# Kernel optimization log

Hardware: AMD Instinct MI355X
Metric: run time of the kernel (lower is better)

The kernel has to match this reference:

```python
import jax, jax.numpy as jnp
import numpy as np

BT = 64  # time chunk size (matches Triton BT)


def _chunk_simple_gla(q, k, v, g):
    """Chunked simple-GLA / RWKV6c forward.
    q,k: [B,H,T,K]; v: [B,H,T,V]; g: [B,H,T] per-token log decay.
    Token-level math: S_t = exp(g_t)*S_{t-1} + k_t v_t^T ; o_t = scale * q_t @ S_t.
    Computed chunk-wise exactly as the Triton kernels do.
    """
    B, H, T, K = q.shape
    V = v.shape[-1]
    NT = T // BT
    scale = K ** -0.5

    qc = q.reshape(B, H, NT, BT, K)
    kc = k.reshape(B, H, NT, BT, K)
    vc = v.reshape(B, H, NT, BT, V)
    gc = jnp.cumsum(g.reshape(B, H, NT, BT), axis=-1)  # chunk-local cumulative log decay
    g_last = gc[..., -1]                               # [B,H,NT]

    # per-chunk kv contribution: sum_s k_s (v_s * exp(g_last - g_s))^T
    w = jnp.exp(g_last[..., None] - gc)                # [B,H,NT,BT]
    chunk_kv = jnp.einsum('bhntk,bhntv->bhnkv', kc, vc * w[..., None])
    decay = jnp.exp(g_last)                            # [B,H,NT]

    # inter-chunk state recurrence: h_n = state BEFORE chunk n
    def scan_fn(S, x):
        d, kv = x
        S_new = d[..., None, None] * S + kv
        return S_new, S  # emit state entering this chunk

    xs = (jnp.moveaxis(decay, 2, 0), jnp.moveaxis(chunk_kv, 2, 0))
    S0 = jnp.zeros((B, H, K, V), dtype=q.dtype)
    _, h = jax.lax.scan(scan_fn, S0, xs)               # h: [NT,B,H,K,V]
    h = jnp.moveaxis(h, 0, 2)                          # [B,H,NT,K,V]

    # inter-chunk output: exp(g_t) * q_t @ h_chunk * scale
    o_inter = jnp.einsum('bhntk,bhnkv->bhntv', qc, h) * jnp.exp(gc)[..., None] * scale

    # intra-chunk causal output with gated mask exp(g_i - g_j), i >= j
    s = jnp.einsum('bhnik,bhnjk->bhnij', qc, kc)
    mask = jnp.tril(jnp.ones((BT, BT), dtype=bool))
    s = jnp.where(mask, s * jnp.exp(gc[..., :, None] - gc[..., None, :]) * scale, 0.0)
    o_intra = jnp.einsum('bhnij,bhnjv->bhniv', s, vc)

    return (o_inter + o_intra).reshape(B, H, T, V)


def setup_inputs() -> dict:
    key = jax.random.key(0)
    kq, kk, kv, kg = jax.random.split(key, 4)
    B, H, T, K, V = 2, 32, 4096, 128, 128
    q = jax.random.normal(kq, (B, H, T, K), dtype=jnp.float32)
    k = jax.random.normal(kk, (B, H, T, K), dtype=jnp.float32)
    v = jax.random.normal(kv, (B, H, T, V), dtype=jnp.float32)
    # log-decay gates: negative so exp(cumsum) is bounded (RWKV6/GLA semantics)
    g = -0.5 * jax.random.uniform(kg, (B, H, T), dtype=jnp.float32)
    return {"q": q, "k": k, "v": v, "g": g}


def reference(q, k, v, g):
    return _chunk_simple_gla(q, k, v, g)
```

## Files before the change

kernel.cpp:

```cpp
#include <hip/hip_runtime.h>
#include <hip/hip_bf16.h>


#define BT 64
#define KD 128
#define VD 128
#define VSG 32
#define NCHUNK 64
#define TLEN 4096
#define SCALE 0.08838834764831845f

#define QSTR 136
#define SHSTR 72
#define SVSTR 136
#define VTSTR 72

typedef __bf16 bf16;
typedef __bf16 bf16x8 __attribute__((ext_vector_type(8)));
typedef __bf16 bf16x4 __attribute__((ext_vector_type(4)));
typedef float f32x4 __attribute__((ext_vector_type(4)));

#define MFMA __builtin_amdgcn_mfma_f32_16x16x32_bf16
#define LGKM_BARRIER() do { asm volatile("s_waitcnt lgkmcnt(0)" ::: "memory"); \
                            __builtin_amdgcn_s_barrier(); } while (0)

__device__ __forceinline__ int ksw(int t) { return ((t >> 3) & 3) << 5; }

__device__ __forceinline__ int vt_off(int vc, int t) {
  int byte = vc * (VTSTR * 2) + t * 2;
  byte ^= ((vc >> 2) & 7) << 4;
  return byte >> 1;
}

__device__ __forceinline__ bf16x8 frag_row(const bf16* p, int stride, int row0,
                                           int kk0, int lane) {
  int row = row0 + (lane & 15);
  int kk = kk0 + ((lane >> 4) << 3);
  return *(const bf16x8*)(p + row * stride + kk);
}

__device__ __forceinline__ bf16x8 krow_frag(const bf16* ks_, int row0, int kk0,
                                            int lane) {
  int row = row0 + (lane & 15);
  int kk = kk0 + ((lane >> 4) << 3);
  int byte = (row * (QSTR * 2) + kk * 2) ^ ksw(row);
  return *(const bf16x8*)((const char*)ks_ + byte);
}

__device__ __forceinline__ bf16x8 kcol_frag(const bf16* ks_, int T0, int kdA) {
  int C = ((T0 >> 3) & 3) << 5;
  int b0 = T0 * (QSTR * 2) + kdA * 2;
  bf16x8 f;
#pragma unroll
  for (int j = 0; j < 8; ++j)
    f[j] = *(const bf16*)((const char*)ks_ + ((b0 + j * (QSTR * 2)) ^ C));
  return f;
}

__device__ __forceinline__ void st4(bf16* p, float a, float b, float c, float d) {
  bf16x4 t;
  t[0] = (bf16)a; t[1] = (bf16)b; t[2] = (bf16)c; t[3] = (bf16)d;
  *(bf16x4*)p = t;
}

__global__ void __launch_bounds__(512, 2)
gla_fused(const float* __restrict__ qg, const float* __restrict__ kg,
          const float* __restrict__ vg, const float* __restrict__ gg,
          float* __restrict__ og)
{
  __shared__ __align__(16) bf16 q_s[2][BT * QSTR];
  __shared__ __align__(16) bf16 k_s[2][BT * QSTR];
  __shared__ __align__(16) bf16 vT_s[3][VSG * VTSTR];
  __shared__ __align__(16) bf16 vwT_s[3][VSG * VTSTR];
  __shared__ __align__(16) bf16 sh_s[2][BT * SHSTR];
  __shared__ __align__(16) bf16 svt_s[2][VSG * SVSTR];
  __shared__ __align__(16) float gc_all[NCHUNK][BT];
  __shared__ float glast_all[NCHUNK];

  const int tid = threadIdx.x;
  const int wave = tid >> 6;
  const int lane = tid & 63;
  const int bh = blockIdx.x & 63;
  const int vseg = blockIdx.x >> 6;

  const int jc = lane & 15;
  const int g4 = lane >> 4;
  const int r0 = g4 << 2;

  const int it = wave & 3;
  const int nt = wave >> 2;
  const int jt0 = (wave < 4) ? 0 : 2;

  const size_t qkbase = (size_t)bh * TLEN * KD;
  const size_t gbase = (size_t)bh * TLEN;
  const size_t vbase = (size_t)bh * TLEN * VD + (size_t)vseg * VSG;
  const int vrow = tid >> 3;
  const int vc0 = (tid & 7) << 2;

  float4 qpf[4], kpf[4], vpf;

  auto loadpf = [&](int n) {
    const float4* q4 = (const float4*)(qg + qkbase + (size_t)n * (BT * KD));
    const float4* k4 = (const float4*)(kg + qkbase + (size_t)n * (BT * KD));
#pragma unroll
    for (int i = 0; i < 4; ++i) { qpf[i] = q4[i * 512 + tid]; kpf[i] = k4[i * 512 + tid]; }
    vpf = *(const float4*)(vg + vbase + (size_t)(n * BT + vrow) * VD + vc0);
  };

  auto stage = [&](int b2, int b3, int n) {
#pragma unroll
    for (int i = 0; i < 4; ++i) {
      int f4 = i * 512 + tid;
      int t = f4 >> 5;
      int kd0 = (f4 & 31) << 2;
      st4(&q_s[b2][t * QSTR + kd0], qpf[i].x, qpf[i].y, qpf[i].z, qpf[i].w);
      int byte = (t * (QSTR * 2) + kd0 * 2) ^ ksw(t);
      st4((bf16*)((char*)k_s[b2] + byte), kpf[i].x, kpf[i].y, kpf[i].z, kpf[i].w);
    }
    bf16* vt = vT_s[b3];
    bf16* vwt = vwT_s[b3];
    float wv = __expf(glast_all[n] - gc_all[n][vrow]);
    vt[vt_off(vc0 + 0, vrow)] = (bf16)vpf.x;
    vt[vt_off(vc0 + 1, vrow)] = (bf16)vpf.y;
    vt[vt_off(vc0 + 2, vrow)] = (bf16)vpf.z;
    vt[vt_off(vc0 + 3, vrow)] = (bf16)vpf.w;
    vwt[vt_off(vc0 + 0, vrow)] = (bf16)(vpf.x * wv);
    vwt[vt_off(vc0 + 1, vrow)] = (bf16)(vpf.y * wv);
    vwt[vt_off(vc0 + 2, vrow)] = (bf16)(vpf.z * wv);
    vwt[vt_off(vc0 + 3, vrow)] = (bf16)(vpf.w * wv);
  };

  auto o_emit = [&](int no, int b2o, int b3o, const bf16x8 (&afp)[4]) {
    f32x4 oacc = {0.f, 0.f, 0.f, 0.f};
#pragma unroll
    for (int ks = 0; ks < 4; ++ks) {
      bf16x8 b = frag_row(svt_s[b2o], SVSTR, nt * 16, ks * 32, lane);
      oacc = MFMA(afp[ks], b, oacc, 0, 0, 0);
    }
    {
      float4 e4 = *(const float4*)&gc_all[no][it * 16 + r0];
      const float* ep = (const float*)&e4;
#pragma unroll
      for (int r = 0; r < 4; ++r) oacc[r] *= __expf(ep[r]) * SCALE;
    }
#pragma unroll
    for (int ks = 0; ks < 2; ++ks) {
      bf16x8 a = frag_row(sh_s[b2o], SHSTR, it * 16, ks * 32, lane);
      bf16x8 b = *(const bf16x8*)(vT_s[b3o] + vt_off(nt * 16 + jc, ks * 32 + (g4 << 3)));
      oacc = MFMA(a, b, oacc, 0, 0, 0);
    }
#pragma unroll
    for (int r = 0; r < 4; ++r) {
      int row = it * 16 + r0 + r;
      og[vbase + (size_t)(no * BT + row) * VD + nt * 16 + jc] = oacc[r];
    }
  };

  f32x4 Sa = {0.f, 0.f, 0.f, 0.f}, Sb = {0.f, 0.f, 0.f, 0.f};
  bf16x8 afp[4];

  loadpf(0);
#pragma unroll 1
  for (int i = 0; i < 8; ++i) {
    int cn = wave * 8 + i;
    float a = gg[gbase + cn * BT + lane];
#pragma unroll
    for (int off = 1; off < 64; off <<= 1) {
      float t = __shfl_up(a, off);
      if (lane >= off) a += t;
    }
    gc_all[cn][lane] = a;
    if (lane == 63) glast_all[cn] = a;
  }
  LGKM_BARRIER();
  stage(0, 0, 0);
  loadpf(1);
  LGKM_BARRIER();

  int b3 = 0;
#pragma unroll 1
  for (int n = 0; n < NCHUNK; ++n) {
    const int b2 = n & 1;
    const int b3n = (b3 == 2) ? 0 : b3 + 1;
    const int b3p = (b3 == 0) ? 2 : b3 - 1;

    if (n > 0) o_emit(n - 1, b2 ^ 1, b3p, afp);

    bf16x8 af[4];
#pragma unroll
    for (int ks = 0; ks < 4; ++ks)
      af[ks] = frag_row(q_s[b2], QSTR, it * 16, ks * 32, lane);

    f32x4 sa0 = {0.f,0.f,0.f,0.f}, sa1 = {0.f,0.f,0.f,0.f};
#pragma unroll
    for (int ks = 0; ks < 4; ++ks) {
      bf16x8 a0 = krow_frag(k_s[b2], jt0 * 16, ks * 32, lane);
      bf16x8 a1 = krow_frag(k_s[b2], (jt0 + 1) * 16, ks * 32, lane);
      sa0 = MFMA(a0, af[ks], sa0, 0, 0, 0);
      sa1 = MFMA(a1, af[ks], sa1, 0, 0, 0);
    }
    {
      int i0 = it * 16 + jc;
      float gci = gc_all[n][i0];
#pragma unroll
      for (int t = 0; t < 2; ++t) {
        f32x4 sv = t ? sa1 : sa0;
        int jb = (jt0 + t) * 16 + r0;
        float4 g4v = *(const float4*)&gc_all[n][jb];
        const float* gj = (const float*)&g4v;
        bf16x4 pk;
#pragma unroll
        for (int r = 0; r < 4; ++r) {
          float val = (i0 >= jb + r) ? sv[r] * __expf(gci - gj[r]) * SCALE : 0.f;
          pk[r] = (bf16)val;
        }
        *(bf16x4*)&sh_s[b2][i0 * SHSTR + jb] = pk;
      }
    }

    st4(&svt_s[b2][jc * SVSTR + wave * 16 + r0], Sa[0], Sa[1], Sa[2], Sa[3]);
    st4(&svt_s[b2][(16 + jc) * SVSTR + wave * 16 + r0], Sb[0], Sb[1], Sb[2], Sb[3]);
    {
      float dec = __expf(glast_all[n]);
#pragma unroll
      for (int r = 0; r < 4; ++r) { Sa[r] *= dec; Sb[r] *= dec; }
#pragma unroll
      for (int ks = 0; ks < 2; ++ks) {
        bf16x8 a = kcol_frag(k_s[b2], ks * 32 + (g4 << 3), wave * 16 + jc);
        bf16x8 b0 = *(const bf16x8*)(vwT_s[b3] + vt_off(jc, ks * 32 + (g4 << 3)));
        bf16x8 b1 = *(const bf16x8*)(vwT_s[b3] + vt_off(16 + jc, ks * 32 + (g4 << 3)));
        Sa = MFMA(a, b0, Sa, 0, 0, 0);
        Sb = MFMA(a, b1, Sb, 0, 0, 0);
      }
    }

    if (n + 1 < NCHUNK) {
      stage(b2 ^ 1, b3n, n + 1);
      if (n + 2 < NCHUNK) loadpf(n + 2);
    }

#pragma unroll
    for (int ks = 0; ks < 4; ++ks) afp[ks] = af[ks];
    b3 = b3n;

    LGKM_BARRIER();
  }

  o_emit(NCHUNK - 1, 1, 0, afp);
}

extern "C" void kernel_launch(void* const* d_in, const int* in_sizes, int n_in,
                              void* d_out, int out_size, void* d_ws, size_t ws_size,
                              hipStream_t stream) {
  const float* q = (const float*)d_in[0];
  const float* k = (const float*)d_in[1];
  const float* v = (const float*)d_in[2];
  const float* g = (const float*)d_in[3];
  float* o = (float*)d_out;
  dim3 grid(256);
  dim3 block(512);
  gla_fused<<<grid, block, 0, stream>>>(q, k, v, g, o);
}
```

Baseline: 161.9 us.

## Split sequence into segments with precomputed segment KV states

```diff
diff --git a/kernel.cpp b/kernel.cpp
--- a/kernel.cpp
+++ b/kernel.cpp
@@ -7,6 +7,7 @@
 #define VD 128
 #define VSG 32
 #define NCHUNK 64
+#define SEGC 16
 #define TLEN 4096
 #define SCALE 0.08838834764831845f
 
@@ -14,6 +15,11 @@
 #define SHSTR 72
 #define SVSTR 136
 #define VTSTR 72
+
+#define KV_PER 16384
+#define KV_TOT (64 * 3 * KV_PER)
+#define GS_OFF KV_TOT
+#define WS_NEED ((size_t)(KV_TOT + 192) * 4)
 
 typedef __bf16 bf16;
 typedef __bf16 bf16x8 __attribute__((ext_vector_type(8)));
@@ -61,6 +67,335 @@
   bf16x4 t;
   t[0] = (bf16)a; t[1] = (bf16)b; t[2] = (bf16)c; t[3] = (bf16)d;
   *(bf16x4*)p = t;
+}
+
+__device__ __forceinline__ void st8(bf16* p, const float4& a, const float4& b) {
+  bf16x8 t;
+  t[0] = (bf16)a.x; t[1] = (bf16)a.y; t[2] = (bf16)a.z; t[3] = (bf16)a.w;
+  t[4] = (bf16)b.x; t[5] = (bf16)b.y; t[6] = (bf16)b.z; t[7] = (bf16)b.w;
+  *(bf16x8*)p = t;
+}
+
+__global__ void __launch_bounds__(512, 2)
+gla_pre(const float* __restrict__ kg, const float* __restrict__ vg,
+        const float* __restrict__ gg, float* __restrict__ ws)
+{
+  __shared__ __align__(16) bf16 k_s[2][BT * QSTR];
+  __shared__ __align__(16) bf16 vwT_s[2][VD * VTSTR];
+  __shared__ __align__(16) float gc_all[SEGC][BT];
+  __shared__ float glast_all[SEGC];
+
+  const int tid = threadIdx.x;
+  const int wave = tid >> 6;
+  const int lane = tid & 63;
+  const int bh = blockIdx.x & 63;
+  const int sub = blockIdx.x >> 6;
+
+  const int jc = lane & 15;
+  const int g4 = lane >> 4;
+  const int r0 = g4 << 2;
+
+  const size_t kbase = (size_t)bh * TLEN * KD + (size_t)sub * 1024 * KD;
+  const size_t gbase = (size_t)bh * TLEN + (size_t)sub * 1024;
+  const int vrow = tid >> 3;
+  const int vcq = (tid & 7) << 2;
+
+  float4 kpf[4], vpf[4];
+
+  auto loadall = [&](int n) {
+    const float4* k4 = (const float4*)(kg + kbase + (size_t)n * (BT * KD));
+    kpf[0] = k4[2 * tid];        kpf[1] = k4[2 * tid + 1];
+    kpf[2] = k4[1024 + 2 * tid]; kpf[3] = k4[1024 + 2 * tid + 1];
+    const float* vrp = vg + kbase + (size_t)(n * BT + vrow) * VD + vcq;
+#pragma unroll
+    for (int q = 0; q < 4; ++q) vpf[q] = *(const float4*)(vrp + q * 32);
+  };
+
+  auto stage = [&](int buf, int n) {
+#pragma unroll
+    for (int i = 0; i < 2; ++i) {
+      int row = i * 32 + (tid >> 4);
+      int col0 = (tid & 15) << 3;
+      int byte = (row * (QSTR * 2) + col0 * 2) ^ ksw(row);
+      st8((bf16*)((char*)k_s[buf] + byte), kpf[2 * i], kpf[2 * i + 1]);
+    }
+    bf16* vwt = vwT_s[buf];
+    float wv = __expf(glast_all[n] - gc_all[n][vrow]);
+#pragma unroll
+    for (int q = 0; q < 4; ++q) {
+      const float* vp = (const float*)&vpf[q];
+#pragma unroll
+      for (int e = 0; e < 4; ++e)
+        vwt[vt_off(vcq + q * 32 + e, vrow)] = (bf16)(vp[e] * wv);
+    }
+  };
+
+  f32x4 S[8];
+#pragma unroll
+  for (int a = 0; a < 8; ++a) S[a] = {0.f, 0.f, 0.f, 0.f};
+
+  loadall(0);
+#pragma unroll 1
+  for (int i = 0; i < 2; ++i) {
+    int cn = wave * 2 + i;
+    float a = gg[gbase + cn * BT + lane];
+#pragma unroll
+    for (int off = 1; off < 64; off <<= 1) {
+      float t = __shfl_up(a, off);
+      if (lane >= off) a += t;
+    }
+    gc_all[cn][lane] = a;
+    if (lane == 63) glast_all[cn] = a;
+  }
+  LGKM_BARRIER();
+  stage(0, 0);
+  loadall(1);
+  LGKM_BARRIER();
+
+#pragma unroll 1
+  for (int n = 0; n < SEGC; ++n) {
+    const int cur = n & 1;
+    float dec = __expf(glast_all[n]);
+#pragma unroll
+    for (int a = 0; a < 8; ++a) S[a] *= dec;
+#pragma unroll
+    for (int ks = 0; ks < 2; ++ks) {
+      bf16x8 ka = kcol_frag(k_s[cur], ks * 32 + (g4 << 3), wave * 16 + jc);
+#pragma unroll
+      for (int a = 0; a < 8; ++a) {
+        bf16x8 b = *(const bf16x8*)(vwT_s[cur] + vt_off(16 * a + jc, ks * 32 + (g4 << 3)));
+        S[a] = MFMA(ka, b, S[a], 0, 0, 0);
+      }
+    }
+    if (n + 1 < SEGC) {
+      stage(cur ^ 1, n + 1);
+      if (n + 2 < SEGC) loadall(n + 2);
+    }
+    LGKM_BARRIER();
+  }
+
+  float* kv = ws + ((size_t)bh * 3 + sub) * KV_PER;
+#pragma unroll
+  for (int a = 0; a < 8; ++a)
+#pragma unroll
+    for (int r = 0; r < 4; ++r)
+      kv[(wave * 16 + r0 + r) * VD + 16 * a + jc] = S[a][r];
+  if (tid == 0) {
+    float gs = 0.f;
+    for (int n = 0; n < SEGC; ++n) gs += glast_all[n];
+    ws[GS_OFF + bh * 3 + sub] = gs;
+  }
+}
+
+__global__ void __launch_bounds__(512, 2)
+gla_main(const float* __restrict__ qg, const float* __restrict__ kg,
+         const float* __restrict__ vg, const float* __restrict__ gg,
+         float* __restrict__ og, const float* __restrict__ ws)
+{
+  __shared__ __align__(16) bf16 q_s[BT * QSTR];
+  __shared__ __align__(16) bf16 k_s[BT * QSTR];
+  __shared__ __align__(16) bf16 vT_s[2][VD * VTSTR];
+  __shared__ __align__(16) bf16 vwT_s[2][VD * VTSTR];
+  __shared__ __align__(16) bf16 sh_s[BT * SHSTR];
+  __shared__ __align__(16) bf16 svt_s[VD * SVSTR];
+  __shared__ __align__(16) float gc_all[SEGC][BT];
+  __shared__ float glast_all[SEGC];
+
+  const int tid = threadIdx.x;
+  const int wave = tid >> 6;
+  const int lane = tid & 63;
+  const int bh = blockIdx.x & 63;
+  const int seg = blockIdx.x >> 6;
+
+  const int jc = lane & 15;
+  const int g4 = lane >> 4;
+  const int r0 = g4 << 2;
+
+  const int it = wave & 3;
+  const int jt0 = (wave < 4) ? 0 : 2;
+  const int vq0 = (wave >> 2) << 2;
+
+  const size_t qkbase = (size_t)bh * TLEN * KD + (size_t)seg * 1024 * KD;
+  const size_t gbase = (size_t)bh * TLEN + (size_t)seg * 1024;
+  const int vrow = tid >> 3;
+  const int vcq = (tid & 7) << 2;
+
+  float4 qpf[4], kpf[4], vpf[4];
+
+  auto loadall = [&](int n) {
+    const float4* q4 = (const float4*)(qg + qkbase + (size_t)n * (BT * KD));
+    const float4* k4 = (const float4*)(kg + qkbase + (size_t)n * (BT * KD));
+    qpf[0] = q4[2 * tid];        qpf[1] = q4[2 * tid + 1];
+    qpf[2] = q4[1024 + 2 * tid]; qpf[3] = q4[1024 + 2 * tid + 1];
+    kpf[0] = k4[2 * tid];        kpf[1] = k4[2 * tid + 1];
+    kpf[2] = k4[1024 + 2 * tid]; kpf[3] = k4[1024 + 2 * tid + 1];
+    const float* vrp = vg + qkbase + (size_t)(n * BT + vrow) * VD + vcq;
+#pragma unroll
+    for (int q = 0; q < 4; ++q) vpf[q] = *(const float4*)(vrp + q * 32);
+  };
+
+  auto stage = [&](int vbuf, int n) {
+#pragma unroll
+    for (int i = 0; i < 2; ++i) {
+      int row = i * 32 + (tid >> 4);
+      int col0 = (tid & 15) << 3;
+      st8(&q_s[row * QSTR + col0], qpf[2 * i], qpf[2 * i + 1]);
+      int byte = (row * (QSTR * 2) + col0 * 2) ^ ksw(row);
+      st8((bf16*)((char*)k_s + byte), kpf[2 * i], kpf[2 * i + 1]);
+    }
+    bf16* vt = vT_s[vbuf];
+    bf16* vwt = vwT_s[vbuf];
+    float wv = __expf(glast_all[n] - gc_all[n][vrow]);
+#pragma unroll
+    for (int q = 0; q < 4; ++q) {
+      const float* vp = (const float*)&vpf[q];
+#pragma unroll
+      for (int e = 0; e < 4; ++e) {
+        int vc = vcq + q * 32 + e;
+        vt[vt_off(vc, vrow)] = (bf16)vp[e];
+        vwt[vt_off(vc, vrow)] = (bf16)(vp[e] * wv);
+      }
+    }
+  };
+
+  f32x4 S[8];
+#pragma unroll
+  for (int a = 0; a < 8; ++a) S[a] = {0.f, 0.f, 0.f, 0.f};
+
+  if (seg > 0) {
+    float D1 = __expf(ws[GS_OFF + bh * 3 + 1]);
+    float D2 = __expf(ws[GS_OFF + bh * 3 + 2]);
+    float mult[3];
+    mult[0] = (seg == 1) ? 1.f : ((seg == 2) ? D1 : D1 * D2);
+    mult[1] = (seg == 2) ? 1.f : D2;
+    mult[2] = 1.f;
+    for (int j = 0; j < seg && j < 3; ++j) {
+      const float* kv = ws + ((size_t)bh * 3 + j) * KV_PER;
+      float m = mult[j];
+#pragma unroll
+      for (int a = 0; a < 8; ++a)
+#pragma unroll
+        for (int r = 0; r < 4; ++r)
+          S[a][r] += m * kv[(wave * 16 + r0 + r) * VD + 16 * a + jc];
+    }
+  }
+
+  loadall(0);
+#pragma unroll 1
+  for (int i = 0; i < 2; ++i) {
+    int cn = wave * 2 + i;
+    float a = gg[gbase + cn * BT + lane];
+#pragma unroll
+    for (int off = 1; off < 64; off <<= 1) {
+      float t = __shfl_up(a, off);
+      if (lane >= off) a += t;
+    }
+    gc_all[cn][lane] = a;
+    if (lane == 63) glast_all[cn] = a;
+  }
+  LGKM_BARRIER();
+  stage(0, 0);
+  loadall(1);
+  LGKM_BARRIER();
+
+#pragma unroll 1
+  for (int n = 0; n < SEGC; ++n) {
+    const int cur = n & 1;
+
+    bf16x8 af[4];
+#pragma unroll
+    for (int ks = 0; ks < 4; ++ks)
+      af[ks] = frag_row(q_s, QSTR, it * 16, ks * 32, lane);
+
+    f32x4 sa0 = {0.f,0.f,0.f,0.f}, sa1 = {0.f,0.f,0.f,0.f};
+#pragma unroll
+    for (int ks = 0; ks < 4; ++ks) {
+      bf16x8 a0 = krow_frag(k_s, jt0 * 16, ks * 32, lane);
+      bf16x8 a1 = krow_frag(k_s, (jt0 + 1) * 16, ks * 32, lane);
+      sa0 = MFMA(a0, af[ks], sa0, 0, 0, 0);
+      sa1 = MFMA(a1, af[ks], sa1, 0, 0, 0);
+    }
+    {
+      int i0 = it * 16 + jc;
+      float gci = gc_all[n][i0];
+#pragma unroll
+      for (int t = 0; t < 2; ++t) {
+        f32x4 sv = t ? sa1 : sa0;
+        int jb = (jt0 + t) * 16 + r0;
+        float4 g4v = *(const float4*)&gc_all[n][jb];
+        const float* gj = (const float*)&g4v;
+        bf16x4 pk;
+#pragma unroll
+        for (int r = 0; r < 4; ++r) {
+          float val = (i0 >= jb + r) ? sv[r] * __expf(gci - gj[r]) * SCALE : 0.f;
+          pk[r] = (bf16)val;
+        }
+        *(bf16x4*)&sh_s[i0 * SHSTR + jb] = pk;
+      }
+    }
+
+#pragma unroll
+    for (int a = 0; a < 8; ++a)
+      st4(&svt_s[(16 * a + jc) * SVSTR + wave * 16 + r0],
+          S[a][0], S[a][1], S[a][2], S[a][3]);
+
+    if (n + 1 < SEGC) {
+      float dec = __expf(glast_all[n]);
+#pragma unroll
+      for (int a = 0; a < 8; ++a) S[a] *= dec;
+#pragma unroll
+      for (int ks = 0; ks < 2; ++ks) {
+        bf16x8 ka = kcol_frag(k_s, ks * 32 + (g4 << 3), wave * 16 + jc);
+#pragma unroll
+        for (int a = 0; a < 8; ++a) {
+          bf16x8 b = *(const bf16x8*)(vwT_s[cur] + vt_off(16 * a + jc, ks * 32 + (g4 << 3)));
+          S[a] = MFMA(ka, b, S[a], 0, 0, 0);
+        }
+      }
+    }
+    LGKM_BARRIER();
+
+    {
+      bf16x8 sha[2];
+#pragma unroll
+      for (int ks = 0; ks < 2; ++ks)
+        sha[ks] = frag_row(sh_s, SHSTR, it * 16, ks * 32, lane);
+      float eg[4];
+      {
+        float4 e4 = *(const float4*)&gc_all[n][it * 16 + r0];
+        const float* ep = (const float*)&e4;
+#pragma unroll
+        for (int r = 0; r < 4; ++r) eg[r] = __expf(ep[r]) * SCALE;
+      }
+#pragma unroll
+      for (int p = 0; p < 4; ++p) {
+        int vq = vq0 + p;
+        f32x4 oacc = {0.f, 0.f, 0.f, 0.f};
+#pragma unroll
+        for (int ks = 0; ks < 4; ++ks) {
+          bf16x8 b = frag_row(svt_s, SVSTR, vq * 16, ks * 32, lane);
+          oacc = MFMA(af[ks], b, oacc, 0, 0, 0);
+        }
+#pragma unroll
+        for (int r = 0; r < 4; ++r) oacc[r] *= eg[r];
+#pragma unroll
+        for (int ks = 0; ks < 2; ++ks) {
+          bf16x8 b = *(const bf16x8*)(vT_s[cur] + vt_off(vq * 16 + jc, ks * 32 + (g4 << 3)));
+          oacc = MFMA(sha[ks], b, oacc, 0, 0, 0);
+        }
+#pragma unroll
+        for (int r = 0; r < 4; ++r) {
+          int row = it * 16 + r0 + r;
+          og[qkbase + (size_t)(n * BT + row) * VD + vq * 16 + jc] = oacc[r];
+        }
+      }
+    }
+    if (n + 1 < SEGC) {
+      stage(cur ^ 1, n + 1);
+      if (n + 2 < SEGC) loadall(n + 2);
+    }
+    LGKM_BARRIER();
+  }
 }
 
 __global__ void __launch_bounds__(512, 2)
@@ -257,7 +592,11 @@
   const float* v = (const float*)d_in[2];
   const float* g = (const float*)d_in[3];
   float* o = (float*)d_out;
-  dim3 grid(256);
-  dim3 block(512);
-  gla_fused<<<grid, block, 0, stream>>>(q, k, v, g, o);
-}
+  if (ws_size >= WS_NEED) {
+    float* ws = (float*)d_ws;
+    gla_pre<<<dim3(192), dim3(512), 0, stream>>>(k, v, g, ws);
+    gla_main<<<dim3(256), dim3(512), 0, stream>>>(q, k, v, g, o, ws);
+  } else {
+    gla_fused<<<dim3(256), dim3(512), 0, stream>>>(q, k, v, g, o);
+  }
+}
```

Result: slower. 171.1 us (median of 2 runs) (+5.6%).
